# Performance work log

Measured on AMD Instinct MI355X. Metric: run time of the kernel, lower is better.

Reference implementation:

```python
import jax, jax.numpy as jnp
import numpy as np

NEMB = 128
N_NODES = 8192
N_EDGES = 16384
N_STEMS = 4096
N_GRAPHS = 256
N_BLOCKS = 105       # BlockDictionary.n_unique_blocks
N_STEMTYPES = 32     # BlockDictionary.n_stem_types
OUT_PER_STEM = 105
OUT_PER_STOP = 1
NUM_CONV_STEPS = 12
SLOPE = 0.01         # nn.LeakyReLU default negative slope


def _act(v):
    return jax.nn.leaky_relu(v, SLOPE)


def setup_inputs() -> dict:
    key = jax.random.key(0)
    ks = jax.random.split(key, 32)
    def p(i, shape, fan_in):
        return jax.random.normal(ks[i], shape, jnp.float32) / np.sqrt(fan_in).astype(np.float32)
    D = NEMB
    inp = {
        "x": jax.random.randint(ks[0], (N_NODES,), 0, N_BLOCKS + 1),
        "stemtypes": jax.random.randint(ks[1], (N_STEMS,), 0, N_STEMTYPES + 1),
        "edge_attr": jax.random.randint(ks[2], (N_EDGES, 2), 0, N_STEMTYPES),
        "edge_index": jax.random.randint(ks[3], (2, N_EDGES), 0, N_NODES),
        "stem_node_idx": jax.random.randint(ks[4], (N_STEMS,), 0, N_NODES),
        "node_batch": jnp.sort(jax.random.randint(ks[5], (N_NODES,), 0, N_GRAPHS)),
        # embedding tables
        "emb_block": p(6, (N_BLOCKS + 1, D), D),
        "emb_stem": p(7, (N_STEMTYPES + 1, D), D),
        "emb_bond": p(8, (N_STEMTYPES, D), D),
        # block2emb MLP
        "b2e_w1": p(9, (D, D), D), "b2e_b1": p(10, (D,), D),
        "b2e_w2": p(11, (D, D), D), "b2e_b2": p(12, (D,), D),
        # NNConv root weight + bias (edge-nn is identity: nn.Sequential())
        "conv_root": p(13, (D, D), D), "conv_bias": p(14, (D,), D),
        # GRU (torch gate order r, z, n)
        "gru_w_ih": p(15, (3 * D, D), D), "gru_w_hh": p(16, (3 * D, D), D),
        "gru_b_ih": p(17, (3 * D,), D), "gru_b_hh": p(18, (3 * D,), D),
        # stem2pred MLP (in = 2*D)
        "s2p_w1": p(19, (D, 2 * D), 2 * D), "s2p_b1": p(20, (D,), 2 * D),
        "s2p_w2": p(21, (D, D), D), "s2p_b2": p(22, (D,), D),
        "s2p_w3": p(23, (OUT_PER_STEM, D), D), "s2p_b3": p(24, (OUT_PER_STEM,), D),
        # global2pred MLP
        "g2p_w1": p(25, (D, D), D), "g2p_b1": p(26, (D,), D),
        "g2p_w2": p(27, (OUT_PER_STOP, D), D), "g2p_b2": p(28, (OUT_PER_STOP,), D),
    }
    return inp


def reference(x, stemtypes, edge_attr, edge_index, stem_node_idx, node_batch,
              emb_block, emb_stem, emb_bond,
              b2e_w1, b2e_b1, b2e_w2, b2e_b2,
              conv_root, conv_bias,
              gru_w_ih, gru_w_hh, gru_b_ih, gru_b_hh,
              s2p_w1, s2p_b1, s2p_w2, s2p_b2, s2p_w3, s2p_b3,
              g2p_w1, g2p_b1, g2p_w2, g2p_b2):
    block_emb = emb_block[x]                          # [N, D]
    stem_emb = emb_stem[stemtypes]                    # [S, D]
    be = emb_bond[edge_attr]                          # [E, 2, D]
    # outer product -> per-edge [D_in, D_out] weight (matches view(-1, in, out))
    W_e = be[:, 0, :, None] * be[:, 1, None, :]       # [E, D, D]

    out = _act(block_emb @ b2e_w1.T + b2e_b1) @ b2e_w2.T + b2e_b2  # [N, D]
    h = out                                           # GRU hidden state

    src, dst = edge_index[0], edge_index[1]
    ones_e = jnp.ones((N_EDGES,), out.dtype)
    deg = jax.ops.segment_sum(ones_e, dst, num_segments=N_NODES)
    inv_deg = jnp.where(deg > 0, 1.0 / jnp.maximum(deg, 1.0), 0.0)[:, None]

    for _ in range(NUM_CONV_STEPS):
        # NNConv: mean_j (x_j @ W_e) + x @ root + bias, then LeakyReLU
        msg = jnp.einsum('ei,eij->ej', out[src], W_e)                  # [E, D]
        agg = jax.ops.segment_sum(msg, dst, num_segments=N_NODES) * inv_deg
        m = _act(agg + out @ conv_root + conv_bias)
        # single-layer GRU, seq_len = 1
        gi = m @ gru_w_ih.T + gru_b_ih
        gh = h @ gru_w_hh.T + gru_b_hh
        ir, iz, inn = jnp.split(gi, 3, axis=-1)
        hr, hz, hn = jnp.split(gh, 3, axis=-1)
        r = jax.nn.sigmoid(ir + hr)
        z = jax.nn.sigmoid(iz + hz)
        n = jnp.tanh(inn + r * hn)
        h = (1.0 - z) * n + z * h
        out = h

    stem_cat = jnp.concatenate([out[stem_node_idx], stem_emb], axis=1)  # [S, 2D]
    s = _act(stem_cat @ s2p_w1.T + s2p_b1)
    s = _act(s @ s2p_w2.T + s2p_b2)
    stem_pred = s @ s2p_w3.T + s2p_b3                                   # [S, out_per_stem]

    # global_mean_pool
    gsum = jax.ops.segment_sum(out, node_batch, num_segments=N_GRAPHS)
    gcnt = jax.ops.segment_sum(jnp.ones((N_NODES,), out.dtype), node_batch, num_segments=N_GRAPHS)
    gmean = gsum / jnp.maximum(gcnt, 1.0)[:, None]
    g = _act(gmean @ g2p_w1.T + g2p_b1)
    stop_pred = g @ g2p_w2.T + g2p_b2                                   # [G, out_per_stop]
    return stem_pred, stop_pred
```

## Files before the change

kernel.cpp:

```cpp
#include <hip/hip_runtime.h>
#include <math.h>

#define D 128
#define NNODES 8192
#define NEDGES 16384
#define NSTEMS 4096
#define NGRAPHS 256
#define NSTEPS 12
#define OPS 105
#define SLOPE 0.01f
#define MT 32
#define NB (NNODES / MT)
#define ECAP 512
#define LDA 136
#define LDA2 264
#define LDQ 40
#define LDH 132

typedef _Float16 half_t;
typedef __attribute__((ext_vector_type(8))) _Float16 f16x8;
typedef __attribute__((ext_vector_type(4))) float f32x4;

__device__ __forceinline__ float leaky(float x) { return x > 0.f ? x : SLOPE * x; }
__device__ __forceinline__ float fast_sigmoid(float x) {
    return __builtin_amdgcn_rcpf(1.f + __expf(-x));
}
__device__ __forceinline__ float fast_tanh(float x) {
    float e = __expf(2.f * x);
    return 1.f - 2.f * __builtin_amdgcn_rcpf(e + 1.f);
}

__device__ __forceinline__ void gbar(int* bar, int sync_no) {
    __syncthreads();
    if (threadIdx.x == 0) {
        int grp = blockIdx.x >> 5;
        int old = __hip_atomic_fetch_add(&bar[grp * 32], 1,
                                         __ATOMIC_RELEASE, __HIP_MEMORY_SCOPE_AGENT);
        if (old == sync_no * 32 - 1) {
            int r = __hip_atomic_fetch_add(&bar[256], 1,
                                           __ATOMIC_RELEASE, __HIP_MEMORY_SCOPE_AGENT);
            if (r == sync_no * 8 - 1)
                __hip_atomic_store(&bar[288], sync_no,
                                   __ATOMIC_RELEASE, __HIP_MEMORY_SCOPE_AGENT);
        }
        while (__hip_atomic_load(&bar[288], __ATOMIC_RELAXED,
                                 __HIP_MEMORY_SCOPE_AGENT) < sync_no)
            __builtin_amdgcn_s_sleep(1);
    }
    __syncthreads();
}

__global__ void k_setup(
    const float* __restrict__ root, const float* __restrict__ wih,
    const float* __restrict__ whh, const float* __restrict__ bond,
    const float* __restrict__ sw1, const float* __restrict__ sw2,
    const float* __restrict__ sw3, const float* __restrict__ bw1,
    const float* __restrict__ bw2, const float* __restrict__ gw1,
    half_t* __restrict__ rootP, half_t* __restrict__ WihP,
    half_t* __restrict__ WhhP, half_t* __restrict__ bondTP,
    half_t* __restrict__ s1P, half_t* __restrict__ s2P, half_t* __restrict__ s3P,
    half_t* __restrict__ w1P, half_t* __restrict__ w2P, half_t* __restrict__ bondQP,
    float* __restrict__ g1T, int* __restrict__ zeroi) {
    int idx = blockIdx.x * 256 + threadIdx.x;
    int which = blockIdx.y;
    if (which == 10) {
        if (idx < 128 * 128) {
            int r = idx >> 7, c = idx & 127;
            g1T[c * 128 + r] = gw1[idx];
        }
        return;
    }
    if (which == 11) {
        if (idx < 512) zeroi[idx] = 0;
        return;
    }
    int KT = (which == 4) ? 8 : (which == 9) ? 1 : 4;
    int NT = (which == 1 || which == 2) ? 24 : (which == 3) ? 2 : (which == 6) ? 7 : 8;
    if (idx >= NT * KT * 512) return;
    int j = idx & 7;
    int L = (idx >> 3) & 63;
    int t = idx >> 9;
    int kt = t % KT, nt = t / KT;
    int k = kt * 32 + (L >> 4) * 8 + j;
    int n = nt * 16 + (L & 15);
    switch (which) {
        case 0: rootP[idx] = (half_t)root[k * D + n]; break;
        case 1: WihP[idx] = (half_t)wih[n * D + k]; break;
        case 2: WhhP[idx] = (half_t)whh[n * D + k]; break;
        case 3: bondTP[idx] = (half_t)bond[n * D + k]; break;
        case 4: s1P[idx] = (half_t)sw1[n * 256 + k]; break;
        case 5: s2P[idx] = (half_t)sw2[n * 128 + k]; break;
        case 6: s3P[idx] = (n < OPS) ? (half_t)sw3[n * 128 + k] : (half_t)0.f; break;
        case 7: w1P[idx] = (half_t)bw1[n * D + k]; break;
        case 8: w2P[idx] = (half_t)bw2[n * D + k]; break;
        case 9: bondQP[idx] = (half_t)bond[k * D + n]; break;
    }
}

__device__ __forceinline__ int lower_bound_dev(const int* a, int n, int v) {
    int lo = 0, hi = n;
    while (lo < hi) {
        int m = (lo + hi) >> 1;
        if (a[m] < v) lo = m + 1;
        else hi = m;
    }
    return lo;
}

__global__ __launch_bounds__(512, 2) void k_fused(
    const int* __restrict__ x, const float* __restrict__ embBlock,
    const half_t* __restrict__ w1P, const float* __restrict__ b1i,
    const half_t* __restrict__ w2P, const float* __restrict__ b2i,
    const half_t* __restrict__ rootP, const half_t* __restrict__ WihP,
    const half_t* __restrict__ WhhP, const half_t* __restrict__ bondTP,
    const half_t* __restrict__ bondQP,
    const float* __restrict__ cbias, const float* __restrict__ bih,
    const float* __restrict__ bhh,
    const int* __restrict__ eidx, const int* __restrict__ eattr,
    float* __restrict__ Pbuf0, float* __restrict__ Pbuf1,
    float* __restrict__ hF,
    const int* __restrict__ sni, const int* __restrict__ stypes,
    const float* __restrict__ embStem,
    const half_t* __restrict__ s1P, const float* __restrict__ sb1,
    const half_t* __restrict__ s2P, const float* __restrict__ sb2,
    const half_t* __restrict__ s3P, const float* __restrict__ sb3,
    const int* __restrict__ batch, const float* __restrict__ g1T,
    const float* __restrict__ gb1, const float* __restrict__ gw2,
    const float* __restrict__ gb2, float* __restrict__ dout,
    int* __restrict__ bar) {
    __shared__ __align__(16) half_t As[MT * LDA];
    __shared__ __align__(16) half_t Am[MT * LDA];
    __shared__ __align__(16) float Hs[MT * LDH];
    __shared__ __align__(16) half_t Qh[MT * LDQ];
    __shared__ __align__(16) float Q[MT * 32];
    __shared__ __align__(16) int4 elist[ECAP];
    __shared__ int degs_s[MT];
    __shared__ int ecnt;

    const int tid = threadIdx.x;
    const int w = tid >> 6;
    const int lane = tid & 63;
    const int quad = lane >> 4;
    const int l16 = lane & 15;
    const int n0 = blockIdx.x * MT;
    const int c = w * 16 + l16;

    if (tid < MT) degs_s[tid] = 0;
    if (tid == 0) ecnt = 0;
    Q[tid] = 0.f;
    Q[tid + 512] = 0.f;
    __syncthreads();

    {
        int row = tid >> 4;
        int col = (tid & 15) * 8;
        const float* src = embBlock + (size_t)x[n0 + row] * D + col;
        float4 v0 = ((const float4*)src)[0];
        float4 v1 = ((const float4*)src)[1];
        f16x8 hv;
        hv[0] = (half_t)v0.x; hv[1] = (half_t)v0.y; hv[2] = (half_t)v0.z; hv[3] = (half_t)v0.w;
        hv[4] = (half_t)v1.x; hv[5] = (half_t)v1.y; hv[6] = (half_t)v1.z; hv[7] = (half_t)v1.w;
        *(f16x8*)&As[row * LDA + col] = hv;
    }
    for (int e = tid; e < NEDGES; e += 512) {
        int dd = eidx[NEDGES + e];
        unsigned r = (unsigned)(dd - n0);
        if (r < MT) {
            int slot = atomicAdd(&ecnt, 1);
            atomicAdd(&degs_s[r], 1);
            if (slot < ECAP) {
                int2 aa = *(const int2*)(eattr + 2 * e);
                elist[slot] = make_int4(eidx[e], aa.x, aa.y, (int)r);
            }
        }
    }
    f16x8 rootB[4], ghB[12], aggB, bondTB[4];
#pragma unroll
    for (int kt = 0; kt < 4; ++kt)
        rootB[kt] = *(const f16x8*)(rootP + (size_t)((w * 4 + kt) * 64 + lane) * 8);
#pragma unroll
    for (int kt = 0; kt < 4; ++kt)
#pragma unroll
        for (int g = 0; g < 3; ++g)
            ghB[g * 4 + kt] = *(const f16x8*)(WhhP + (size_t)(((g * 8 + w) * 4 + kt) * 64 + lane) * 8);
    aggB = *(const f16x8*)(bondQP + (size_t)(w * 64 + lane) * 8);
    {
        const int ntb = w & 1;
#pragma unroll
        for (int kt = 0; kt < 4; ++kt)
            bondTB[kt] = *(const f16x8*)(bondTP + (size_t)((ntb * 4 + kt) * 64 + lane) * 8);
    }
    const float cb = cbias[c];
    const float bi0 = bih[c], bi1 = bih[D + c], bi2 = bih[2 * D + c];
    const float bh0 = bhh[c], bh1 = bhh[D + c], bh2 = bhh[2 * D + c];
    __syncthreads();

    int4 ep = make_int4(0, 0, 0, 0);
    float idg = 0.f;
    const int m = min(ecnt, ECAP);
    const bool have = (tid < m);
    if (have) {
        ep = elist[tid];
        idg = 1.0f / (float)degs_s[ep.w];
    }

    {
        f32x4 acc[2] = {{0.f, 0.f, 0.f, 0.f}, {0.f, 0.f, 0.f, 0.f}};
#pragma unroll
        for (int kt = 0; kt < 4; ++kt) {
            f16x8 b = *(const f16x8*)(w1P + (size_t)((w * 4 + kt) * 64 + lane) * 8);
            f16x8 a0 = *(const f16x8*)&As[(0 + l16) * LDA + kt * 32 + quad * 8];
            f16x8 a1 = *(const f16x8*)&As[(16 + l16) * LDA + kt * 32 + quad * 8];
            acc[0] = __builtin_amdgcn_mfma_f32_16x16x32_f16(a0, b, acc[0], 0, 0, 0);
            acc[1] = __builtin_amdgcn_mfma_f32_16x16x32_f16(a1, b, acc[1], 0, 0, 0);
        }
        float bb = b1i[c];
#pragma unroll
        for (int mt = 0; mt < 2; ++mt)
#pragma unroll
            for (int r = 0; r < 4; ++r)
                Am[(mt * 16 + quad * 4 + r) * LDA + c] = (half_t)leaky(acc[mt][r] + bb);
    }
    __syncthreads();
    {
        f32x4 acc[2] = {{0.f, 0.f, 0.f, 0.f}, {0.f, 0.f, 0.f, 0.f}};
#pragma unroll
        for (int kt = 0; kt < 4; ++kt) {
            f16x8 b = *(const f16x8*)(w2P + (size_t)((w * 4 + kt) * 64 + lane) * 8);
            f16x8 a0 = *(const f16x8*)&Am[(0 + l16) * LDA + kt * 32 + quad * 8];
            f16x8 a1 = *(const f16x8*)&Am[(16 + l16) * LDA + kt * 32 + quad * 8];
            acc[0] = __builtin_amdgcn_mfma_f32_16x16x32_f16(a0, b, acc[0], 0, 0, 0);
            acc[1] = __builtin_amdgcn_mfma_f32_16x16x32_f16(a1, b, acc[1], 0, 0, 0);
        }
        float bb = b2i[c];
#pragma unroll
        for (int mt = 0; mt < 2; ++mt)
#pragma unroll
            for (int r = 0; r < 4; ++r) {
                int row = mt * 16 + quad * 4 + r;
                float h = acc[mt][r] + bb;
                Hs[row * LDH + c] = h;
                As[row * LDA + c] = (half_t)h;
            }
    }
    __syncthreads();
    if (w < 4) {
        int mt = w >> 1;
        f32x4 acc = {0.f, 0.f, 0.f, 0.f};
#pragma unroll
        for (int kt = 0; kt < 4; ++kt) {
            f16x8 a = *(const f16x8*)&As[(mt * 16 + l16) * LDA + kt * 32 + quad * 8];
            acc = __builtin_amdgcn_mfma_f32_16x16x32_f16(a, bondTB[kt], acc, 0, 0, 0);
        }
#pragma unroll
        for (int r = 0; r < 4; ++r)
            __hip_atomic_store(
                &Pbuf0[(size_t)(n0 + mt * 16 + quad * 4 + r) * 32 + (w & 1) * 16 + l16],
                acc[r], __ATOMIC_RELAXED, __HIP_MEMORY_SCOPE_AGENT);
    }
    int sync_no = 1;
    gbar(bar, sync_no);

    float* Pp = Pbuf0;
    float* Pn = Pbuf1;
    for (int step = 0; step < NSTEPS; ++step) {
        float wv = 0.f;
        if (have)
            wv = __hip_atomic_load(&Pp[(size_t)ep.x * 32 + ep.y],
                                   __ATOMIC_RELAXED, __HIP_MEMORY_SCOPE_AGENT) * idg;
        f32x4 convAcc[2] = {{0.f, 0.f, 0.f, 0.f}, {0.f, 0.f, 0.f, 0.f}};
#pragma unroll
        for (int kt = 0; kt < 4; ++kt) {
            f16x8 a0 = *(const f16x8*)&As[(0 + l16) * LDA + kt * 32 + quad * 8];
            f16x8 a1 = *(const f16x8*)&As[(16 + l16) * LDA + kt * 32 + quad * 8];
            convAcc[0] = __builtin_amdgcn_mfma_f32_16x16x32_f16(a0, rootB[kt], convAcc[0], 0, 0, 0);
            convAcc[1] = __builtin_amdgcn_mfma_f32_16x16x32_f16(a1, rootB[kt], convAcc[1], 0, 0, 0);
        }
        if (have) atomicAdd(&Q[ep.w * 32 + ep.z], wv);
        f32x4 ghA[2][3];
#pragma unroll
        for (int mt = 0; mt < 2; ++mt)
#pragma unroll
            for (int g = 0; g < 3; ++g) ghA[mt][g] = f32x4{0.f, 0.f, 0.f, 0.f};
#pragma unroll
        for (int kt = 0; kt < 4; ++kt) {
            f16x8 a0 = *(const f16x8*)&As[(0 + l16) * LDA + kt * 32 + quad * 8];
            f16x8 a1 = *(const f16x8*)&As[(16 + l16) * LDA + kt * 32 + quad * 8];
#pragma unroll
            for (int g = 0; g < 3; ++g) {
                ghA[0][g] = __builtin_amdgcn_mfma_f32_16x16x32_f16(a0, ghB[g * 4 + kt], ghA[0][g], 0, 0, 0);
                ghA[1][g] = __builtin_amdgcn_mfma_f32_16x16x32_f16(a1, ghB[g * 4 + kt], ghA[1][g], 0, 0, 0);
            }
        }
        __syncthreads();

        f16x8 giB[12];
#pragma unroll
        for (int kt = 0; kt < 4; ++kt)
#pragma unroll
            for (int g = 0; g < 3; ++g)
                giB[g * 4 + kt] = *(const f16x8*)(WihP + (size_t)(((g * 8 + w) * 4 + kt) * 64 + lane) * 8);

        Qh[(tid >> 5) * LDQ + (tid & 31)] = (half_t)Q[tid];
        Qh[((tid + 512) >> 5) * LDQ + (tid & 31)] = (half_t)Q[tid + 512];
        __syncthreads();
        Q[tid] = 0.f;
        Q[tid + 512] = 0.f;

#pragma unroll
        for (int mt = 0; mt < 2; ++mt) {
            f32x4 acc = {0.f, 0.f, 0.f, 0.f};
            f16x8 a = *(const f16x8*)&Qh[(mt * 16 + l16) * LDQ + quad * 8];
            acc = __builtin_amdgcn_mfma_f32_16x16x32_f16(a, aggB, acc, 0, 0, 0);
#pragma unroll
            for (int r = 0; r < 4; ++r) {
                float mm = convAcc[mt][r] + cb + acc[r];
                Am[(mt * 16 + quad * 4 + r) * LDA + c] = (half_t)leaky(mm);
            }
        }
        __syncthreads();

        f32x4 giA[2][3];
#pragma unroll
        for (int mt = 0; mt < 2; ++mt)
#pragma unroll
            for (int g = 0; g < 3; ++g) giA[mt][g] = f32x4{0.f, 0.f, 0.f, 0.f};
#pragma unroll
        for (int kt = 0; kt < 4; ++kt) {
            f16x8 a0 = *(const f16x8*)&Am[(0 + l16) * LDA + kt * 32 + quad * 8];
            f16x8 a1 = *(const f16x8*)&Am[(16 + l16) * LDA + kt * 32 + quad * 8];
#pragma unroll
            for (int g = 0; g < 3; ++g) {
                giA[0][g] = __builtin_amdgcn_mfma_f32_16x16x32_f16(a0, giB[g * 4 + kt], giA[0][g], 0, 0, 0);
                giA[1][g] = __builtin_amdgcn_mfma_f32_16x16x32_f16(a1, giB[g * 4 + kt], giA[1][g], 0, 0, 0);
            }
        }
#pragma unroll
        for (int mt = 0; mt < 2; ++mt) {
#pragma unroll
            for (int r = 0; r < 4; ++r) {
                int row = mt * 16 + quad * 4 + r;
                float rg = fast_sigmoid(giA[mt][0][r] + bi0 + ghA[mt][0][r] + bh0);
                float z = fast_sigmoid(giA[mt][1][r] + bi1 + ghA[mt][1][r] + bh1);
                float nn = fast_tanh(giA[mt][2][r] + bi2 + rg * (ghA[mt][2][r] + bh2));
                float hnew = (1.f - z) * nn + z * Hs[row * LDH + c];
                Hs[row * LDH + c] = hnew;
                As[row * LDA + c] = (half_t)hnew;
            }
        }
        __syncthreads();

        if (step < NSTEPS - 1) {
            if (w < 4) {
                int mt = w >> 1;
                f32x4 acc = {0.f, 0.f, 0.f, 0.f};
#pragma unroll
                for (int kt = 0; kt < 4; ++kt) {
                    f16x8 a = *(const f16x8*)&As[(mt * 16 + l16) * LDA + kt * 32 + quad * 8];
                    acc = __builtin_amdgcn_mfma_f32_16x16x32_f16(a, bondTB[kt], acc, 0, 0, 0);
                }
#pragma unroll
                for (int r = 0; r < 4; ++r)
                    __hip_atomic_store(
                        &Pn[(size_t)(n0 + mt * 16 + quad * 4 + r) * 32 + (w & 1) * 16 + l16],
                        acc[r], __ATOMIC_RELAXED, __HIP_MEMORY_SCOPE_AGENT);
            }
            ++sync_no;
            gbar(bar, sync_no);
            float* tsw = Pp; Pp = Pn; Pn = tsw;
        }
    }

    {
        int row = tid >> 4;
        int col = (tid & 15) * 8;
        const unsigned long long* s8 = (const unsigned long long*)&Hs[row * LDH + col];
        unsigned long long* d8 = (unsigned long long*)(hF + (size_t)(n0 + row) * D + col);
#pragma unroll
        for (int q2 = 0; q2 < 4; ++q2)
            __hip_atomic_store(d8 + q2, s8[q2], __ATOMIC_RELAXED, __HIP_MEMORY_SCOPE_AGENT);
    }
    ++sync_no;
    gbar(bar, sync_no);

    half_t* cat = As;
    half_t* t1 = Am;
    half_t* t2 = Am + 16 * LDA;
    const int s0 = blockIdx.x * 16;
    {
        int row = tid >> 5;
        int col = (tid & 31) * 8;
        const float* src;
        if (col < D) src = hF + (size_t)sni[s0 + row] * D + col;
        else src = embStem + (size_t)stypes[s0 + row] * D + (col - D);
        float4 v0 = ((const float4*)src)[0];
        float4 v1 = ((const float4*)src)[1];
        f16x8 hv;
        hv[0] = (half_t)v0.x; hv[1] = (half_t)v0.y; hv[2] = (half_t)v0.z; hv[3] = (half_t)v0.w;
        hv[4] = (half_t)v1.x; hv[5] = (half_t)v1.y; hv[6] = (half_t)v1.z; hv[7] = (half_t)v1.w;
        *(f16x8*)&cat[row * LDA2 + col] = hv;
    }
    __syncthreads();
    {
        f32x4 acc = {0.f, 0.f, 0.f, 0.f};
#pragma unroll
        for (int kt = 0; kt < 8; ++kt) {
            f16x8 b = *(const f16x8*)(s1P + (size_t)((w * 8 + kt) * 64 + lane) * 8);
            f16x8 a = *(const f16x8*)&cat[l16 * LDA2 + kt * 32 + quad * 8];
            acc = __builtin_amdgcn_mfma_f32_16x16x32_f16(a, b, acc, 0, 0, 0);
        }
        float bb = sb1[c];
#pragma unroll
        for (int r = 0; r < 4; ++r)
            t1[(quad * 4 + r) * LDA + c] = (half_t)leaky(acc[r] + bb);
    }
    __syncthreads();
    {
        f32x4 acc = {0.f, 0.f, 0.f, 0.f};
#pragma unroll
        for (int kt = 0; kt < 4; ++kt) {
            f16x8 b = *(const f16x8*)(s2P + (size_t)((w * 4 + kt) * 64 + lane) * 8);
            f16x8 a = *(const f16x8*)&t1[l16 * LDA + kt * 32 + quad * 8];
            acc = __builtin_amdgcn_mfma_f32_16x16x32_f16(a, b, acc, 0, 0, 0);
        }
        float bb = sb2[c];
#pragma unroll
        for (int r = 0; r < 4; ++r)
            t2[(quad * 4 + r) * LDA + c] = (half_t)leaky(acc[r] + bb);
    }
    __syncthreads();
    if (w < 7) {
        f32x4 acc = {0.f, 0.f, 0.f, 0.f};
#pragma unroll
        for (int kt = 0; kt < 4; ++kt) {
            f16x8 b = *(const f16x8*)(s3P + (size_t)((w * 4 + kt) * 64 + lane) * 8);
            f16x8 a = *(const f16x8*)&t2[l16 * LDA + kt * 32 + quad * 8];
            acc = __builtin_amdgcn_mfma_f32_16x16x32_f16(a, b, acc, 0, 0, 0);
        }
        int j = w * 16 + l16;
        if (j < OPS) {
            float bb = sb3[j];
#pragma unroll
            for (int r = 0; r < 4; ++r)
                dout[(size_t)(s0 + quad * 4 + r) * OPS + j] = acc[r] + bb;
        }
    }

    {
        const int g = blockIdx.x;
        const int j = tid & 127;
        const int grp = tid >> 7;
        float* part = Q;
        float* mean_s = Q + 512;
        float* red = Q + 640;
        int lo = lower_bound_dev(batch, NNODES, g);
        int hi = lower_bound_dev(batch, NNODES, g + 1);
        float sum = 0.f;
        for (int n = lo + grp; n < hi; n += 4) sum += hF[(size_t)n * D + j];
        part[grp * 128 + j] = sum;
        __syncthreads();
        if (grp == 0) {
            float denom = (hi > lo) ? (float)(hi - lo) : 1.0f;
            mean_s[j] = (part[j] + part[128 + j] + part[256 + j] + part[384 + j]) / denom;
        }
        __syncthreads();
        float a = 0.f;
        for (int i = grp * 32; i < grp * 32 + 32; ++i) a += mean_s[i] * g1T[i * D + j];
        part[grp * 128 + j] = a;
        __syncthreads();
        if (grp == 0) {
            float aa = part[j] + part[128 + j] + part[256 + j] + part[384 + j] + gb1[j];
            red[j] = leaky(aa) * gw2[j];
        }
        __syncthreads();
        for (int off = 64; off > 0; off >>= 1) {
            if (tid < off) red[tid] += red[tid + off];
            __syncthreads();
        }
        if (tid == 0) dout[NSTEMS * OPS + g] = red[0] + gb2[0];
    }
}

extern "C" void kernel_launch(void* const* d_in, const int* in_sizes, int n_in,
                              void* d_out, int out_size, void* d_ws, size_t ws_size,
                              hipStream_t stream) {
    const int* x = (const int*)d_in[0];
    const int* stypes = (const int*)d_in[1];
    const int* eattr = (const int*)d_in[2];
    const int* eidx = (const int*)d_in[3];
    const int* sni = (const int*)d_in[4];
    const int* batch = (const int*)d_in[5];
    const float* embBlock = (const float*)d_in[6];
    const float* embStem = (const float*)d_in[7];
    const float* embBond = (const float*)d_in[8];
    const float* b2e_w1 = (const float*)d_in[9];
    const float* b2e_b1 = (const float*)d_in[10];
    const float* b2e_w2 = (const float*)d_in[11];
    const float* b2e_b2 = (const float*)d_in[12];
    const float* conv_root = (const float*)d_in[13];
    const float* conv_bias = (const float*)d_in[14];
    const float* gru_w_ih = (const float*)d_in[15];
    const float* gru_w_hh = (const float*)d_in[16];
    const float* gru_b_ih = (const float*)d_in[17];
    const float* gru_b_hh = (const float*)d_in[18];
    const float* s2p_w1 = (const float*)d_in[19];
    const float* s2p_b1 = (const float*)d_in[20];
    const float* s2p_w2 = (const float*)d_in[21];
    const float* s2p_b2 = (const float*)d_in[22];
    const float* s2p_w3 = (const float*)d_in[23];
    const float* s2p_b3 = (const float*)d_in[24];
    const float* g2p_w1 = (const float*)d_in[25];
    const float* g2p_b1 = (const float*)d_in[26];
    const float* g2p_w2 = (const float*)d_in[27];
    const float* g2p_b2 = (const float*)d_in[28];
    float* out_f = (float*)d_out;

    float* W = (float*)d_ws;
    size_t off = 0;
    auto alloc = [&](size_t words) {
        size_t o = off;
        off += (words + 3) & ~(size_t)3;
        return o;
    };
    float* hF = W + alloc(NNODES * D);
    float* P0 = W + alloc(NNODES * 32);
    float* P1 = W + alloc(NNODES * 32);
    half_t* rootP = (half_t*)(W + alloc(16384 / 2));
    half_t* WihP = (half_t*)(W + alloc(49152 / 2));
    half_t* WhhP = (half_t*)(W + alloc(49152 / 2));
    half_t* bondTP = (half_t*)(W + alloc(4096 / 2));
    half_t* s1P = (half_t*)(W + alloc(32768 / 2));
    half_t* s2P = (half_t*)(W + alloc(16384 / 2));
    half_t* s3P = (half_t*)(W + alloc(14336 / 2));
    half_t* w1P = (half_t*)(W + alloc(16384 / 2));
    half_t* w2P = (half_t*)(W + alloc(16384 / 2));
    half_t* bondQP = (half_t*)(W + alloc(4096 / 2));
    float* g1T = W + alloc(128 * 128);
    int* bar = (int*)(W + alloc(512));

    k_setup<<<dim3(192, 12), 256, 0, stream>>>(
        conv_root, gru_w_ih, gru_w_hh, embBond, s2p_w1, s2p_w2, s2p_w3,
        b2e_w1, b2e_w2, g2p_w1,
        rootP, WihP, WhhP, bondTP, s1P, s2P, s3P, w1P, w2P, bondQP,
        g1T, bar);

    k_fused<<<NB, 512, 0, stream>>>(
        x, embBlock,
        w1P, b2e_b1, w2P, b2e_b2,
        rootP, WihP, WhhP, bondTP, bondQP,
        conv_bias, gru_b_ih, gru_b_hh,
        eidx, eattr,
        P0, P1, hF,
        sni, stypes, embStem,
        s1P, s2p_b1, s2P, s2p_b2, s3P, s2p_b3,
        batch, g1T, g2p_b1, g2p_w2, g2p_b2,
        out_f, bar);
}
```

Measured before the change: 224.0 us.

## Replace hierarchical grid barrier with split arrive/wait flags and overlap independent work

Swaps the two-level atomic-counter grid barrier for per-block monotonic flags. Each block publishes its step number with a release store, and one wavefront polls all 256 flags using a wave-wide vote. Arrive is split from wait, so the hidden-state GRU matmul (which needs no neighbour data) and the stem-embedding half of the first stem MLP layer run before waiting. This is meant to shorten the serialized barrier chain and hide barrier latency behind work that does not depend on it, at the cost of every block polling 256 flags on each step.

```diff
diff --git a/kernel.cpp b/kernel.cpp
--- a/kernel.cpp
+++ b/kernel.cpp
@@ -30,22 +30,22 @@
     return 1.f - 2.f * __builtin_amdgcn_rcpf(e + 1.f);
 }
 
-__device__ __forceinline__ void gbar(int* bar, int sync_no) {
-    __syncthreads();
-    if (threadIdx.x == 0) {
-        int grp = blockIdx.x >> 5;
-        int old = __hip_atomic_fetch_add(&bar[grp * 32], 1,
-                                         __ATOMIC_RELEASE, __HIP_MEMORY_SCOPE_AGENT);
-        if (old == sync_no * 32 - 1) {
-            int r = __hip_atomic_fetch_add(&bar[256], 1,
-                                           __ATOMIC_RELEASE, __HIP_MEMORY_SCOPE_AGENT);
-            if (r == sync_no * 8 - 1)
-                __hip_atomic_store(&bar[288], sync_no,
-                                   __ATOMIC_RELEASE, __HIP_MEMORY_SCOPE_AGENT);
-        }
-        while (__hip_atomic_load(&bar[288], __ATOMIC_RELAXED,
-                                 __HIP_MEMORY_SCOPE_AGENT) < sync_no)
+__device__ __forceinline__ void arrive_flag(int* pflag, int sync_no) {
+    __hip_atomic_store(&pflag[blockIdx.x], sync_no, __ATOMIC_RELEASE,
+                       __HIP_MEMORY_SCOPE_AGENT);
+}
+__device__ __forceinline__ void wait_all(int* pflag, int sync_no) {
+    if (threadIdx.x < 64) {
+        const int base = threadIdx.x * 4;
+        for (;;) {
+            int a = __hip_atomic_load(&pflag[base + 0], __ATOMIC_RELAXED, __HIP_MEMORY_SCOPE_AGENT);
+            int b = __hip_atomic_load(&pflag[base + 1], __ATOMIC_RELAXED, __HIP_MEMORY_SCOPE_AGENT);
+            int c = __hip_atomic_load(&pflag[base + 2], __ATOMIC_RELAXED, __HIP_MEMORY_SCOPE_AGENT);
+            int d = __hip_atomic_load(&pflag[base + 3], __ATOMIC_RELAXED, __HIP_MEMORY_SCOPE_AGENT);
+            int ok = (a >= sync_no) & (b >= sync_no) & (c >= sync_no) & (d >= sync_no);
+            if (__all(ok)) break;
             __builtin_amdgcn_s_sleep(1);
+        }
     }
     __syncthreads();
 }
@@ -127,7 +127,7 @@
     const int* __restrict__ batch, const float* __restrict__ g1T,
     const float* __restrict__ gb1, const float* __restrict__ gw2,
     const float* __restrict__ gb2, float* __restrict__ dout,
-    int* __restrict__ bar) {
+    int* __restrict__ pflag) {
     __shared__ __align__(16) half_t As[MT * LDA];
     __shared__ __align__(16) half_t Am[MT * LDA];
     __shared__ __align__(16) float Hs[MT * LDH];
@@ -258,12 +258,28 @@
                 &Pbuf0[(size_t)(n0 + mt * 16 + quad * 4 + r) * 32 + (w & 1) * 16 + l16],
                 acc[r], __ATOMIC_RELAXED, __HIP_MEMORY_SCOPE_AGENT);
     }
-    int sync_no = 1;
-    gbar(bar, sync_no);
+    __syncthreads();
+    if (tid == 0) arrive_flag(pflag, 1);
 
     float* Pp = Pbuf0;
     float* Pn = Pbuf1;
     for (int step = 0; step < NSTEPS; ++step) {
+        f32x4 ghA[2][3];
+#pragma unroll
+        for (int mt = 0; mt < 2; ++mt)
+#pragma unroll
+            for (int g = 0; g < 3; ++g) ghA[mt][g] = f32x4{0.f, 0.f, 0.f, 0.f};
+#pragma unroll
+        for (int kt = 0; kt < 4; ++kt) {
+            f16x8 a0 = *(const f16x8*)&As[(0 + l16) * LDA + kt * 32 + quad * 8];
+            f16x8 a1 = *(const f16x8*)&As[(16 + l16) * LDA + kt * 32 + quad * 8];
+#pragma unroll
+            for (int g = 0; g < 3; ++g) {
+                ghA[0][g] = __builtin_amdgcn_mfma_f32_16x16x32_f16(a0, ghB[g * 4 + kt], ghA[0][g], 0, 0, 0);
+                ghA[1][g] = __builtin_amdgcn_mfma_f32_16x16x32_f16(a1, ghB[g * 4 + kt], ghA[1][g], 0, 0, 0);
+            }
+        }
+        wait_all(pflag, step + 1);
         float wv = 0.f;
         if (have)
             wv = __hip_atomic_load(&Pp[(size_t)ep.x * 32 + ep.y],
@@ -277,21 +293,6 @@
             convAcc[1] = __builtin_amdgcn_mfma_f32_16x16x32_f16(a1, rootB[kt], convAcc[1], 0, 0, 0);
         }
         if (have) atomicAdd(&Q[ep.w * 32 + ep.z], wv);
-        f32x4 ghA[2][3];
-#pragma unroll
-        for (int mt = 0; mt < 2; ++mt)
-#pragma unroll
-            for (int g = 0; g < 3; ++g) ghA[mt][g] = f32x4{0.f, 0.f, 0.f, 0.f};
-#pragma unroll
-        for (int kt = 0; kt < 4; ++kt) {
-            f16x8 a0 = *(const f16x8*)&As[(0 + l16) * LDA + kt * 32 + quad * 8];
-            f16x8 a1 = *(const f16x8*)&As[(16 + l16) * LDA + kt * 32 + quad * 8];
-#pragma unroll
-            for (int g = 0; g < 3; ++g) {
-                ghA[0][g] = __builtin_amdgcn_mfma_f32_16x16x32_f16(a0, ghB[g * 4 + kt], ghA[0][g], 0, 0, 0);
-                ghA[1][g] = __builtin_amdgcn_mfma_f32_16x16x32_f16(a1, ghB[g * 4 + kt], ghA[1][g], 0, 0, 0);
-            }
-        }
         __syncthreads();
 
         f16x8 giB[12];
@@ -365,12 +366,16 @@
                         &Pn[(size_t)(n0 + mt * 16 + quad * 4 + r) * 32 + (w & 1) * 16 + l16],
                         acc[r], __ATOMIC_RELAXED, __HIP_MEMORY_SCOPE_AGENT);
             }
-            ++sync_no;
-            gbar(bar, sync_no);
+            __syncthreads();
+            if (tid == 0) arrive_flag(pflag, step + 2);
             float* tsw = Pp; Pp = Pn; Pn = tsw;
         }
     }
 
+    half_t* cat = As;
+    half_t* t1 = Am;
+    half_t* t2 = Am + 16 * LDA;
+    const int s0 = blockIdx.x * 16;
     {
         int row = tid >> 4;
         int col = (tid & 15) * 8;
@@ -380,19 +385,33 @@
         for (int q2 = 0; q2 < 4; ++q2)
             __hip_atomic_store(d8 + q2, s8[q2], __ATOMIC_RELAXED, __HIP_MEMORY_SCOPE_AGENT);
     }
-    ++sync_no;
-    gbar(bar, sync_no);
-
-    half_t* cat = As;
-    half_t* t1 = Am;
-    half_t* t2 = Am + 16 * LDA;
-    const int s0 = blockIdx.x * 16;
-    {
-        int row = tid >> 5;
-        int col = (tid & 31) * 8;
-        const float* src;
-        if (col < D) src = hF + (size_t)sni[s0 + row] * D + col;
-        else src = embStem + (size_t)stypes[s0 + row] * D + (col - D);
+    if (tid < 256) {
+        int row = tid >> 4;
+        int col = (tid & 15) * 8;
+        const float* src = embStem + (size_t)stypes[s0 + row] * D + col;
+        float4 v0 = ((const float4*)src)[0];
+        float4 v1 = ((const float4*)src)[1];
+        f16x8 hv;
+        hv[0] = (half_t)v0.x; hv[1] = (half_t)v0.y; hv[2] = (half_t)v0.z; hv[3] = (half_t)v0.w;
+        hv[4] = (half_t)v1.x; hv[5] = (half_t)v1.y; hv[6] = (half_t)v1.z; hv[7] = (half_t)v1.w;
+        *(f16x8*)&cat[row * LDA2 + 128 + col] = hv;
+    }
+    __syncthreads();
+    if (tid == 0) arrive_flag(pflag, NSTEPS + 1);
+
+    f32x4 accS = {0.f, 0.f, 0.f, 0.f};
+#pragma unroll
+    for (int kt = 4; kt < 8; ++kt) {
+        f16x8 b = *(const f16x8*)(s1P + (size_t)((w * 8 + kt) * 64 + lane) * 8);
+        f16x8 a = *(const f16x8*)&cat[l16 * LDA2 + kt * 32 + quad * 8];
+        accS = __builtin_amdgcn_mfma_f32_16x16x32_f16(a, b, accS, 0, 0, 0);
+    }
+    wait_all(pflag, NSTEPS + 1);
+
+    if (tid < 256) {
+        int row = tid >> 4;
+        int col = (tid & 15) * 8;
+        const float* src = hF + (size_t)sni[s0 + row] * D + col;
         float4 v0 = ((const float4*)src)[0];
         float4 v1 = ((const float4*)src)[1];
         f16x8 hv;
@@ -402,17 +421,16 @@
     }
     __syncthreads();
     {
-        f32x4 acc = {0.f, 0.f, 0.f, 0.f};
-#pragma unroll
-        for (int kt = 0; kt < 8; ++kt) {
+#pragma unroll
+        for (int kt = 0; kt < 4; ++kt) {
             f16x8 b = *(const f16x8*)(s1P + (size_t)((w * 8 + kt) * 64 + lane) * 8);
             f16x8 a = *(const f16x8*)&cat[l16 * LDA2 + kt * 32 + quad * 8];
-            acc = __builtin_amdgcn_mfma_f32_16x16x32_f16(a, b, acc, 0, 0, 0);
+            accS = __builtin_amdgcn_mfma_f32_16x16x32_f16(a, b, accS, 0, 0, 0);
         }
         float bb = sb1[c];
 #pragma unroll
         for (int r = 0; r < 4; ++r)
-            t1[(quad * 4 + r) * LDA + c] = (half_t)leaky(acc[r] + bb);
+            t1[(quad * 4 + r) * LDA + c] = (half_t)leaky(accS[r] + bb);
     }
     __syncthreads();
     {
@@ -536,13 +554,13 @@
     half_t* w2P = (half_t*)(W + alloc(16384 / 2));
     half_t* bondQP = (half_t*)(W + alloc(4096 / 2));
     float* g1T = W + alloc(128 * 128);
-    int* bar = (int*)(W + alloc(512));
+    int* pflag = (int*)(W + alloc(512));
 
     k_setup<<<dim3(192, 12), 256, 0, stream>>>(
         conv_root, gru_w_ih, gru_w_hh, embBond, s2p_w1, s2p_w2, s2p_w3,
         b2e_w1, b2e_w2, g2p_w1,
         rootP, WihP, WhhP, bondTP, s1P, s2P, s3P, w1P, w2P, bondQP,
-        g1T, bar);
+        g1T, pflag);
 
     k_fused<<<NB, 512, 0, stream>>>(
         x, embBlock,
@@ -554,5 +572,5 @@
         sni, stypes, embStem,
         s1P, s2p_b1, s2P, s2p_b2, s3P, s2p_b3,
         batch, g1T, g2p_b1, g2p_w2, g2p_b2,
-        out_f, bar);
-}
+        out_f, pflag);
+}
```

Result: slower. 264.1 us (+17.9%).
